# Kernel optimization log

Hardware: AMD Instinct MI355X
Metric: run time of the kernel (lower is better)

## Reference

```python
import jax, jax.numpy as jnp
import numpy as np

ALPHA, BETA, GAMMA = 1.0, 0.5, 0.1
IGNORE = 255


def setup_inputs() -> dict:
    key = jax.random.key(0)
    k1, k2, k3 = jax.random.split(key, 3)
    n, c, h, w, d = 8, 21, 512, 512, 32
    logit = jax.random.normal(k1, (n, c, h, w), dtype=jnp.float32)
    target = jax.random.randint(k2, (n, 1, h, w), 0, 21, dtype=jnp.int32)
    features_in = jax.random.normal(k3, (n, h * w, d), dtype=jnp.float32)
    return {"logit": logit, "target": target, "features_in": features_in}


def reference(logit, target, features_in):
    n, c, h, w = logit.shape
    P = h * w  # total_size per image (sum of all label counts incl. ignore)
    lab = target.reshape(n, P)
    valid = lab != IGNORE
    lab_safe = jnp.where(valid, lab, 0)
    vm = valid.astype(logit.dtype)

    # --- CE loss (mean over non-ignored pixels, as torch CrossEntropyLoss) ---
    logp = jax.nn.log_softmax(logit, axis=1).transpose(0, 2, 3, 1).reshape(n, P, c)
    ce_pix = -jnp.take_along_axis(logp, lab_safe[..., None], axis=2)[..., 0]
    CE = jnp.sum(ce_pix * vm) / jnp.maximum(jnp.sum(vm), 1.0)

    # --- per-pixel logit terms (VAR / Inter), vectorized over the python loop ---
    logit_f = logit.transpose(0, 2, 3, 1).reshape(n, P, c)  # [n,P,c]
    lg = jnp.take_along_axis(logit_f, lab_safe[..., None], axis=2)[..., 0]  # logit at own label
    VAR = jnp.sum(-lg * vm) / P
    Inter = jnp.sum((jnp.sum(logit_f, axis=-1) - lg) * vm) / P

    # --- Center loss: per-image per-class variance of features_in (segment reduce) ---
    onehot = jax.nn.one_hot(lab_safe, c, dtype=logit.dtype) * vm[..., None]  # [n,P,c]
    counts = jnp.sum(onehot, axis=1)                                    # [n,c]
    sums = jnp.einsum('npc,npd->ncd', onehot, features_in)              # class sums
    sumsq = jnp.einsum('npc,np->nc', onehot, jnp.sum(features_in ** 2, axis=-1))
    # sum ||f - mean||^2 = sum||f||^2 - ||sum f||^2 / count
    mean_term = jnp.sum(sums ** 2, axis=-1) / jnp.maximum(counts, 1.0)
    Center = jnp.sum(jnp.where(counts > 0, sumsq - mean_term, 0.0)) / P

    loss = (CE + ALPHA * VAR + BETA * Inter + GAMMA * Center) / n
    return loss
```

## Files before the change

kernel.cpp:

```cpp
#include <hip/hip_runtime.h>


constexpr int   N_IMG  = 8;
constexpr int   C_CLS  = 21;
constexpr int   P_PIX  = 512 * 512;
constexpr int   PQ     = P_PIX / 4;
constexpr int   IGN    = 255;
constexpr float ALPHA  = 1.0f, BETA = 0.5f, GAMMA = 0.1f;

constexpr int MAIN_BLOCKS = 1024;
constexpr int PX_BLK      = 2048;
constexpr int TILE_PX     = 64;
constexpr int NT          = PX_BLK / TILE_PX;

constexpr int OFF_PIX  = 0;
constexpr int OFF_SSQ  = OFF_PIX + MAIN_BLOCKS * 4;
constexpr int OFF_CLS  = OFF_SSQ + MAIN_BLOCKS;
constexpr int OFF_CNT  = OFF_CLS + MAIN_BLOCKS * 672;
constexpr int OFF_MEAN = OFF_CNT + MAIN_BLOCKS * C_CLS;

__device__ __forceinline__ void gl_lds16(const float* g, void* l)
{
    __builtin_amdgcn_global_load_lds(
        (const __attribute__((address_space(1))) void*)g,
        (__attribute__((address_space(3))) void*)l, 16, 0, 0);
}

__global__ __launch_bounds__(256, 4) void main_kernel(
    const float* __restrict__ logit, const int* __restrict__ target,
    const float* __restrict__ feats, float* __restrict__ ws)
{
    __shared__ __align__(16) char smem[24 * 1024];
    __shared__ int   s_hist[C_CLS];
    __shared__ float s_red[4][4];
    __shared__ float s_ssq[4];

    int* s_lab = (int*)smem;

    const int tid   = threadIdx.x;
    const int img   = blockIdx.x >> 7;
    const int chunk = blockIdx.x & 127;
    const int p0    = chunk * PX_BLK;

    const float* fbase = feats + ((size_t)img * P_PIX + p0) * 32;

    if (tid < C_CLS) s_hist[tid] = 0;
    __syncthreads();

    {
        gl_lds16(fbase + (size_t)tid * 4,
                 smem + 8192 + (size_t)(tid & ~63) * 16);
        gl_lds16(fbase + (size_t)(256 + tid) * 4,
                 smem + 8192 + (size_t)((256 + tid) & ~63) * 16);
    }

    float ce = 0.f, vm = 0.f, var = 0.f, inter = 0.f;

#pragma unroll 1
    for (int qi = 0; qi < 2; ++qi) {
        const int pq = chunk * 512 + qi * 256 + tid;
        const int4 t = ((const int4*)target)[(size_t)img * PQ + pq];
        const float4* lp = (const float4*)logit + (size_t)img * C_CLS * PQ + pq;

        ((int4*)s_lab)[qi * 256 + tid] = t;

        float4 s  = {0.f, 0.f, 0.f, 0.f};
        float4 sc = {0.f, 0.f, 0.f, 0.f};
        float4 lg = {0.f, 0.f, 0.f, 0.f};

#pragma unroll 1
        for (int cb = 0; cb < C_CLS; cb += 7) {
            float4 x[7];
#pragma unroll
            for (int i = 0; i < 7; ++i) x[i] = lp[(size_t)(cb + i) * PQ];
#pragma unroll
            for (int i = 0; i < 7; ++i) {
                const int ch = cb + i;
                const float4 v = x[i];
                s.x += __expf(v.x); s.y += __expf(v.y);
                s.z += __expf(v.z); s.w += __expf(v.w);
                sc.x += v.x; sc.y += v.y; sc.z += v.z; sc.w += v.w;
                lg.x = (t.x == ch) ? v.x : lg.x;
                lg.y = (t.y == ch) ? v.y : lg.y;
                lg.z = (t.z == ch) ? v.z : lg.z;
                lg.w = (t.w == ch) ? v.w : lg.w;
            }
        }

        if (t.x != IGN) atomicAdd(&s_hist[t.x], 1);
        if (t.y != IGN) atomicAdd(&s_hist[t.y], 1);
        if (t.z != IGN) atomicAdd(&s_hist[t.z], 1);
        if (t.w != IGN) atomicAdd(&s_hist[t.w], 1);

        {
            const float v = (t.x != IGN) ? 1.f : 0.f;
            vm += v; ce += v * (__logf(s.x) - lg.x); var -= v * lg.x; inter += v * (sc.x - lg.x);
        }
        {
            const float v = (t.y != IGN) ? 1.f : 0.f;
            vm += v; ce += v * (__logf(s.y) - lg.y); var -= v * lg.y; inter += v * (sc.y - lg.y);
        }
        {
            const float v = (t.z != IGN) ? 1.f : 0.f;
            vm += v; ce += v * (__logf(s.z) - lg.z); var -= v * lg.z; inter += v * (sc.z - lg.z);
        }
        {
            const float v = (t.w != IGN) ? 1.f : 0.f;
            vm += v; ce += v * (__logf(s.w) - lg.w); var -= v * lg.w; inter += v * (sc.w - lg.w);
        }
    }

    for (int off = 32; off; off >>= 1) {
        ce    += __shfl_xor(ce, off);
        vm    += __shfl_xor(vm, off);
        var   += __shfl_xor(var, off);
        inter += __shfl_xor(inter, off);
    }
    const int wv = tid >> 6;
    if ((tid & 63) == 0) {
        s_red[wv][0] = ce; s_red[wv][1] = vm; s_red[wv][2] = var; s_red[wv][3] = inter;
    }
    __syncthreads();

    if (tid < 4) {
        ws[OFF_PIX + blockIdx.x * 4 + tid] =
            s_red[0][tid] + s_red[1][tid] + s_red[2][tid] + s_red[3][tid];
    }
    if (tid < C_CLS) {
        ((int*)ws)[OFF_CNT + blockIdx.x * C_CLS + tid] = s_hist[tid];
    }

    const int pl = tid >> 3;
    const int dg = tid & 7;

    float4 acc[C_CLS];
#pragma unroll
    for (int c = 0; c < C_CLS; ++c) acc[c] = {0.f, 0.f, 0.f, 0.f};
    float ssq = 0.f;

#pragma unroll 1
    for (int tt = 0; tt < NT; ++tt) {
        const float* cur = (const float*)(smem + 8192 + (size_t)(tt & 1) * 8192);
        if (tt + 1 < NT) {
            char* nxt = smem + 8192 + (size_t)((tt + 1) & 1) * 8192;
            const float* g = fbase + (size_t)(tt + 1) * TILE_PX * 32;
            gl_lds16(g + (size_t)tid * 4,         nxt + (size_t)(tid & ~63) * 16);
            gl_lds16(g + (size_t)(256 + tid) * 4, nxt + (size_t)((256 + tid) & ~63) * 16);
            asm volatile("s_waitcnt vmcnt(2)" ::: "memory");
        } else {
            asm volatile("s_waitcnt vmcnt(0)" ::: "memory");
        }
        __builtin_amdgcn_s_barrier();

#pragma unroll
        for (int h = 0; h < 2; ++h) {
            const int lp2 = h * 32 + pl;
            const int lab = s_lab[tt * TILE_PX + lp2];
            const float4 f = ((const float4*)cur)[lp2 * 8 + dg];
            const float vld = (lab != IGN) ? 1.f : 0.f;
            ssq += vld * (f.x * f.x + f.y * f.y + f.z * f.z + f.w * f.w);
#pragma unroll
            for (int c = 0; c < C_CLS; ++c) {
                const float m = (lab == c) ? 1.f : 0.f;
                acc[c].x += m * f.x; acc[c].y += m * f.y;
                acc[c].z += m * f.z; acc[c].w += m * f.w;
            }
        }
        __builtin_amdgcn_s_barrier();
    }

    __syncthreads();

#pragma unroll
    for (int c = 0; c < C_CLS; ++c) {
        for (int off = 8; off <= 32; off <<= 1) {
            acc[c].x += __shfl_xor(acc[c].x, off);
            acc[c].y += __shfl_xor(acc[c].y, off);
            acc[c].z += __shfl_xor(acc[c].z, off);
            acc[c].w += __shfl_xor(acc[c].w, off);
        }
    }
    for (int off = 1; off < 64; off <<= 1) ssq += __shfl_xor(ssq, off);

    float4* s_part = (float4*)smem;
    if ((tid & 63) < 8) {
#pragma unroll
        for (int c = 0; c < C_CLS; ++c) s_part[(wv * 8 + dg) * C_CLS + c] = acc[c];
    }
    if ((tid & 63) == 0) s_ssq[wv] = ssq;
    __syncthreads();

    if (tid < C_CLS * 8) {
        const int c = tid >> 3, g = tid & 7;
        const float4 a = s_part[(0 * 8 + g) * C_CLS + c];
        const float4 b = s_part[(1 * 8 + g) * C_CLS + c];
        const float4 d = s_part[(2 * 8 + g) * C_CLS + c];
        const float4 e = s_part[(3 * 8 + g) * C_CLS + c];
        float4 v;
        v.x = a.x + b.x + d.x + e.x;
        v.y = a.y + b.y + d.y + e.y;
        v.z = a.z + b.z + d.z + e.z;
        v.w = a.w + b.w + d.w + e.w;
        ((float4*)(ws + OFF_CLS))[(size_t)blockIdx.x * 168 + tid] = v;
    }
    if (tid == 0)
        ws[OFF_SSQ + blockIdx.x] = s_ssq[0] + s_ssq[1] + s_ssq[2] + s_ssq[3];
}

__global__ __launch_bounds__(128) void reduce_kernel(float* __restrict__ ws)
{
    __shared__ float sred[128];
    __shared__ int   s_cnt;

    const int img = blockIdx.x / C_CLS;
    const int c   = blockIdx.x % C_CLS;
    const int tid = threadIdx.x;
    const int d   = tid & 31;
    const int qq  = tid >> 5;

    if (tid == 0) s_cnt = 0;
    __syncthreads();

    {
        const int* cp = (const int*)ws + OFF_CNT;
        const int cnt = cp[(img * 128 + tid) * C_CLS + c];
        atomicAdd(&s_cnt, cnt);
    }

    float s = 0.f;
    for (int b = qq; b < 128; b += 4)
        s += ws[OFF_CLS + (size_t)(img * 128 + b) * 672 + c * 32 + d];
    sred[tid] = s;
    __syncthreads();
    if (tid < 64) sred[tid] += sred[tid + 64];
    __syncthreads();
    if (tid < 32) {
        const float Sd = sred[tid] + sred[tid + 32];
        float n2 = Sd * Sd;
        for (int off = 1; off < 32; off <<= 1) n2 += __shfl_xor(n2, off);
        if (tid == 0)
            ws[OFF_MEAN + blockIdx.x] = n2 / fmaxf((float)s_cnt, 1.f);
    }
}

__global__ __launch_bounds__(256) void finalize_kernel(
    const float* __restrict__ ws, float* __restrict__ out)
{
    __shared__ float fr[4][6];
    const int tid = threadIdx.x;

    float ce = 0.f, vm = 0.f, var = 0.f, inter = 0.f, ssq = 0.f, mean = 0.f;
    for (int b = tid; b < MAIN_BLOCKS; b += 256) {
        const float* p = ws + OFF_PIX + b * 4;
        ce += p[0]; vm += p[1]; var += p[2]; inter += p[3];
        ssq += ws[OFF_SSQ + b];
    }
    if (tid < N_IMG * C_CLS) mean = ws[OFF_MEAN + tid];

    for (int off = 32; off; off >>= 1) {
        ce   += __shfl_xor(ce, off);   vm    += __shfl_xor(vm, off);
        var  += __shfl_xor(var, off);  inter += __shfl_xor(inter, off);
        ssq  += __shfl_xor(ssq, off);  mean  += __shfl_xor(mean, off);
    }
    const int wv = tid >> 6;
    if ((tid & 63) == 0) {
        fr[wv][0] = ce;  fr[wv][1] = vm;   fr[wv][2] = var;
        fr[wv][3] = inter; fr[wv][4] = ssq; fr[wv][5] = mean;
    }
    __syncthreads();
    if (tid == 0) {
        const float CE_s  = fr[0][0] + fr[1][0] + fr[2][0] + fr[3][0];
        const float VM    = fr[0][1] + fr[1][1] + fr[2][1] + fr[3][1];
        const float VAR_s = fr[0][2] + fr[1][2] + fr[2][2] + fr[3][2];
        const float INT_s = fr[0][3] + fr[1][3] + fr[2][3] + fr[3][3];
        const float SSQ   = fr[0][4] + fr[1][4] + fr[2][4] + fr[3][4];
        const float MEAN  = fr[0][5] + fr[1][5] + fr[2][5] + fr[3][5];
        const float invP   = 1.f / (float)P_PIX;
        const float CE     = CE_s / fmaxf(VM, 1.f);
        const float VAR    = VAR_s * invP;
        const float Inter  = INT_s * invP;
        const float Center = (SSQ - MEAN) * invP;
        out[0] = (CE + ALPHA * VAR + BETA * Inter + GAMMA * Center) / (float)N_IMG;
    }
}

extern "C" void kernel_launch(void* const* d_in, const int* in_sizes, int n_in,
                              void* d_out, int out_size, void* d_ws, size_t ws_size,
                              hipStream_t stream)
{
    const float* logit  = (const float*)d_in[0];
    const int*   target = (const int*)d_in[1];
    const float* feats  = (const float*)d_in[2];
    float* ws  = (float*)d_ws;
    float* out = (float*)d_out;

    main_kernel    <<<MAIN_BLOCKS, 256, 0, stream>>>(logit, target, feats, ws);
    reduce_kernel  <<<N_IMG * C_CLS, 128, 0, stream>>>(ws);
    finalize_kernel<<<1, 256, 0, stream>>>(ws, out);
}
```

Before: 511.0 us.

## Double block threads and split class accumulators across thread pairs

The main kernel goes from 256 to 512 threads per block, so each thread handles one pixel quad instead of two. All 21 logit channel loads are issued up front, raising memory-level parallelism. In the feature segment-reduce, each thread pair splits the 21 class accumulators by even/odd class, cutting per-thread accumulator registers roughly in half so more waves fit. The cost is extra cross-wave reduction work, and the higher launch bound may cause register spills.

```diff
diff --git a/kernel.cpp b/kernel.cpp
--- a/kernel.cpp
+++ b/kernel.cpp
@@ -26,66 +26,58 @@
         (__attribute__((address_space(3))) void*)l, 16, 0, 0);
 }
 
-__global__ __launch_bounds__(256, 4) void main_kernel(
+__global__ __launch_bounds__(512, 8) void main_kernel(
     const float* __restrict__ logit, const int* __restrict__ target,
     const float* __restrict__ feats, float* __restrict__ ws)
 {
     __shared__ __align__(16) char smem[24 * 1024];
     __shared__ int   s_hist[C_CLS];
-    __shared__ float s_red[4][4];
-    __shared__ float s_ssq[4];
+    __shared__ float s_red[8][4];
+    __shared__ float s_ssq[8];
 
     int* s_lab = (int*)smem;
 
     const int tid   = threadIdx.x;
     const int img   = blockIdx.x >> 7;
     const int chunk = blockIdx.x & 127;
-    const int p0    = chunk * PX_BLK;
-
-    const float* fbase = feats + ((size_t)img * P_PIX + p0) * 32;
+    const int wv    = tid >> 6;
+
+    const float* fbase = feats + ((size_t)img * P_PIX + chunk * PX_BLK) * 32;
 
     if (tid < C_CLS) s_hist[tid] = 0;
     __syncthreads();
 
+    gl_lds16(fbase + (size_t)tid * 4, smem + 8192 + (size_t)(tid & ~63) * 16);
+
+    float ce = 0.f, vm = 0.f, var = 0.f, inter = 0.f;
     {
-        gl_lds16(fbase + (size_t)tid * 4,
-                 smem + 8192 + (size_t)(tid & ~63) * 16);
-        gl_lds16(fbase + (size_t)(256 + tid) * 4,
-                 smem + 8192 + (size_t)((256 + tid) & ~63) * 16);
-    }
-
-    float ce = 0.f, vm = 0.f, var = 0.f, inter = 0.f;
-
-#pragma unroll 1
-    for (int qi = 0; qi < 2; ++qi) {
-        const int pq = chunk * 512 + qi * 256 + tid;
+        const int pq = chunk * 512 + tid;
         const int4 t = ((const int4*)target)[(size_t)img * PQ + pq];
+        ((int4*)s_lab)[tid] = t;
         const float4* lp = (const float4*)logit + (size_t)img * C_CLS * PQ + pq;
-
-        ((int4*)s_lab)[qi * 256 + tid] = t;
 
         float4 s  = {0.f, 0.f, 0.f, 0.f};
         float4 sc = {0.f, 0.f, 0.f, 0.f};
         float4 lg = {0.f, 0.f, 0.f, 0.f};
 
-#pragma unroll 1
-        for (int cb = 0; cb < C_CLS; cb += 7) {
-            float4 x[7];
-#pragma unroll
-            for (int i = 0; i < 7; ++i) x[i] = lp[(size_t)(cb + i) * PQ];
-#pragma unroll
-            for (int i = 0; i < 7; ++i) {
-                const int ch = cb + i;
-                const float4 v = x[i];
-                s.x += __expf(v.x); s.y += __expf(v.y);
-                s.z += __expf(v.z); s.w += __expf(v.w);
-                sc.x += v.x; sc.y += v.y; sc.z += v.z; sc.w += v.w;
-                lg.x = (t.x == ch) ? v.x : lg.x;
-                lg.y = (t.y == ch) ? v.y : lg.y;
-                lg.z = (t.z == ch) ? v.z : lg.z;
-                lg.w = (t.w == ch) ? v.w : lg.w;
-            }
-        }
+#define LOADX(i) const float4 x##i = lp[(size_t)(i) * PQ];
+        LOADX(0)  LOADX(1)  LOADX(2)  LOADX(3)  LOADX(4)  LOADX(5)  LOADX(6)
+        LOADX(7)  LOADX(8)  LOADX(9)  LOADX(10) LOADX(11) LOADX(12) LOADX(13)
+        LOADX(14) LOADX(15) LOADX(16) LOADX(17) LOADX(18) LOADX(19) LOADX(20)
+#undef LOADX
+
+#define CONS(i) { const float4 v = x##i;                                   \
+        s.x += __expf(v.x); s.y += __expf(v.y);                            \
+        s.z += __expf(v.z); s.w += __expf(v.w);                            \
+        sc.x += v.x; sc.y += v.y; sc.z += v.z; sc.w += v.w;                \
+        lg.x = (t.x == (i)) ? v.x : lg.x;                                  \
+        lg.y = (t.y == (i)) ? v.y : lg.y;                                  \
+        lg.z = (t.z == (i)) ? v.z : lg.z;                                  \
+        lg.w = (t.w == (i)) ? v.w : lg.w; }
+        CONS(0)  CONS(1)  CONS(2)  CONS(3)  CONS(4)  CONS(5)  CONS(6)
+        CONS(7)  CONS(8)  CONS(9)  CONS(10) CONS(11) CONS(12) CONS(13)
+        CONS(14) CONS(15) CONS(16) CONS(17) CONS(18) CONS(19) CONS(20)
+#undef CONS
 
         if (t.x != IGN) atomicAdd(&s_hist[t.x], 1);
         if (t.y != IGN) atomicAdd(&s_hist[t.y], 1);
@@ -116,95 +108,104 @@
         var   += __shfl_xor(var, off);
         inter += __shfl_xor(inter, off);
     }
-    const int wv = tid >> 6;
     if ((tid & 63) == 0) {
         s_red[wv][0] = ce; s_red[wv][1] = vm; s_red[wv][2] = var; s_red[wv][3] = inter;
     }
     __syncthreads();
 
-    if (tid < 4) {
-        ws[OFF_PIX + blockIdx.x * 4 + tid] =
-            s_red[0][tid] + s_red[1][tid] + s_red[2][tid] + s_red[3][tid];
-    }
-    if (tid < C_CLS) {
-        ((int*)ws)[OFF_CNT + blockIdx.x * C_CLS + tid] = s_hist[tid];
-    }
-
-    const int pl = tid >> 3;
-    const int dg = tid & 7;
-
-    float4 acc[C_CLS];
-#pragma unroll
-    for (int c = 0; c < C_CLS; ++c) acc[c] = {0.f, 0.f, 0.f, 0.f};
+    const int half = tid & 1;
+    const int dg   = (tid >> 1) & 7;
+    const int pxg  = tid >> 4;
+
+#define DEFACC(k) float4 a##k = {0.f, 0.f, 0.f, 0.f};
+    DEFACC(0) DEFACC(1) DEFACC(2) DEFACC(3) DEFACC(4) DEFACC(5)
+    DEFACC(6) DEFACC(7) DEFACC(8) DEFACC(9) DEFACC(10)
+#undef DEFACC
     float ssq = 0.f;
 
 #pragma unroll 1
     for (int tt = 0; tt < NT; ++tt) {
         const float* cur = (const float*)(smem + 8192 + (size_t)(tt & 1) * 8192);
         if (tt + 1 < NT) {
-            char* nxt = smem + 8192 + (size_t)((tt + 1) & 1) * 8192;
-            const float* g = fbase + (size_t)(tt + 1) * TILE_PX * 32;
-            gl_lds16(g + (size_t)tid * 4,         nxt + (size_t)(tid & ~63) * 16);
-            gl_lds16(g + (size_t)(256 + tid) * 4, nxt + (size_t)((256 + tid) & ~63) * 16);
-            asm volatile("s_waitcnt vmcnt(2)" ::: "memory");
+            gl_lds16(fbase + (size_t)(tt + 1) * TILE_PX * 32 + (size_t)tid * 4,
+                     smem + 8192 + (size_t)((tt + 1) & 1) * 8192
+                          + (size_t)(tid & ~63) * 16);
+            asm volatile("s_waitcnt vmcnt(1)" ::: "memory");
         } else {
             asm volatile("s_waitcnt vmcnt(0)" ::: "memory");
         }
+        __builtin_amdgcn_sched_barrier(0);
         __builtin_amdgcn_s_barrier();
+        __builtin_amdgcn_sched_barrier(0);
 
 #pragma unroll
         for (int h = 0; h < 2; ++h) {
-            const int lp2 = h * 32 + pl;
-            const int lab = s_lab[tt * TILE_PX + lp2];
-            const float4 f = ((const float4*)cur)[lp2 * 8 + dg];
-            const float vld = (lab != IGN) ? 1.f : 0.f;
-            ssq += vld * (f.x * f.x + f.y * f.y + f.z * f.z + f.w * f.w);
+            const int px  = h * 32 + pxg;
+            const int lab = s_lab[tt * TILE_PX + px];
+            const float4 f = ((const float4*)cur)[px * 8 + dg];
+            const int labh = lab - half;
+            const float vss = (half == 0 && lab != IGN) ? 1.f : 0.f;
+            ssq += vss * (f.x * f.x + f.y * f.y + f.z * f.z + f.w * f.w);
+#define STEP(k) { const float m = (labh == (2 * (k))) ? 1.f : 0.f;         \
+            a##k.x += m * f.x; a##k.y += m * f.y;                          \
+            a##k.z += m * f.z; a##k.w += m * f.w; }
+            STEP(0) STEP(1) STEP(2) STEP(3) STEP(4) STEP(5)
+            STEP(6) STEP(7) STEP(8) STEP(9) STEP(10)
+#undef STEP
+        }
+        __builtin_amdgcn_sched_barrier(0);
+        __builtin_amdgcn_s_barrier();
+    }
+
+    __syncthreads();
+
+#define REDACC(k)                                                          \
+    a##k.x += __shfl_xor(a##k.x, 16); a##k.x += __shfl_xor(a##k.x, 32);    \
+    a##k.y += __shfl_xor(a##k.y, 16); a##k.y += __shfl_xor(a##k.y, 32);    \
+    a##k.z += __shfl_xor(a##k.z, 16); a##k.z += __shfl_xor(a##k.z, 32);    \
+    a##k.w += __shfl_xor(a##k.w, 16); a##k.w += __shfl_xor(a##k.w, 32);
+    REDACC(0) REDACC(1) REDACC(2) REDACC(3) REDACC(4) REDACC(5)
+    REDACC(6) REDACC(7) REDACC(8) REDACC(9) REDACC(10)
+#undef REDACC
+    for (int off = 1; off < 64; off <<= 1) ssq += __shfl_xor(ssq, off);
+
+    float4* s_part = (float4*)smem;
+    if ((tid & 48) == 0) {
+        const int pbase = (wv * 8 + dg) * C_CLS;
+#define STORE(k) s_part[pbase + 2 * (k) + half] = a##k;
+        STORE(0) STORE(1) STORE(2) STORE(3) STORE(4) STORE(5)
+        STORE(6) STORE(7) STORE(8) STORE(9)
+        if (half == 0) { STORE(10) }
+#undef STORE
+    }
+    if ((tid & 63) == 0) s_ssq[wv] = ssq;
+    __syncthreads();
+
+    if (tid < 4) {
+        float r = 0.f;
 #pragma unroll
-            for (int c = 0; c < C_CLS; ++c) {
-                const float m = (lab == c) ? 1.f : 0.f;
-                acc[c].x += m * f.x; acc[c].y += m * f.y;
-                acc[c].z += m * f.z; acc[c].w += m * f.w;
-            }
-        }
-        __builtin_amdgcn_s_barrier();
-    }
-
-    __syncthreads();
-
-#pragma unroll
-    for (int c = 0; c < C_CLS; ++c) {
-        for (int off = 8; off <= 32; off <<= 1) {
-            acc[c].x += __shfl_xor(acc[c].x, off);
-            acc[c].y += __shfl_xor(acc[c].y, off);
-            acc[c].z += __shfl_xor(acc[c].z, off);
-            acc[c].w += __shfl_xor(acc[c].w, off);
-        }
-    }
-    for (int off = 1; off < 64; off <<= 1) ssq += __shfl_xor(ssq, off);
-
-    float4* s_part = (float4*)smem;
-    if ((tid & 63) < 8) {
-#pragma unroll
-        for (int c = 0; c < C_CLS; ++c) s_part[(wv * 8 + dg) * C_CLS + c] = acc[c];
-    }
-    if ((tid & 63) == 0) s_ssq[wv] = ssq;
-    __syncthreads();
-
+        for (int w = 0; w < 8; ++w) r += s_red[w][tid];
+        ws[OFF_PIX + blockIdx.x * 4 + tid] = r;
+    }
+    if (tid < C_CLS) {
+        ((int*)ws)[OFF_CNT + blockIdx.x * C_CLS + tid] = s_hist[tid];
+    }
     if (tid < C_CLS * 8) {
         const int c = tid >> 3, g = tid & 7;
-        const float4 a = s_part[(0 * 8 + g) * C_CLS + c];
-        const float4 b = s_part[(1 * 8 + g) * C_CLS + c];
-        const float4 d = s_part[(2 * 8 + g) * C_CLS + c];
-        const float4 e = s_part[(3 * 8 + g) * C_CLS + c];
-        float4 v;
-        v.x = a.x + b.x + d.x + e.x;
-        v.y = a.y + b.y + d.y + e.y;
-        v.z = a.z + b.z + d.z + e.z;
-        v.w = a.w + b.w + d.w + e.w;
+        float4 v = {0.f, 0.f, 0.f, 0.f};
+#pragma unroll
+        for (int w = 0; w < 8; ++w) {
+            const float4 p = s_part[(w * 8 + g) * C_CLS + c];
+            v.x += p.x; v.y += p.y; v.z += p.z; v.w += p.w;
+        }
         ((float4*)(ws + OFF_CLS))[(size_t)blockIdx.x * 168 + tid] = v;
     }
-    if (tid == 0)
-        ws[OFF_SSQ + blockIdx.x] = s_ssq[0] + s_ssq[1] + s_ssq[2] + s_ssq[3];
+    if (tid == 0) {
+        float r = 0.f;
+#pragma unroll
+        for (int w = 0; w < 8; ++w) r += s_ssq[w];
+        ws[OFF_SSQ + blockIdx.x] = r;
+    }
 }
 
 __global__ __launch_bounds__(128) void reduce_kernel(float* __restrict__ ws)
@@ -294,7 +295,7 @@
     float* ws  = (float*)d_ws;
     float* out = (float*)d_out;
 
-    main_kernel    <<<MAIN_BLOCKS, 256, 0, stream>>>(logit, target, feats, ws);
+    main_kernel    <<<MAIN_BLOCKS, 512, 0, stream>>>(logit, target, feats, ws);
     reduce_kernel  <<<N_IMG * C_CLS, 128, 0, stream>>>(ws);
     finalize_kernel<<<1, 256, 0, stream>>>(ws, out);
 }
```

Result: slower. 562.0 us (+10.0%).
